# Performance work log

Hardware: AMD Instinct MI355X
Metric: run time of the kernel (lower is better)

The kernel has to match this reference:

```python
import jax, jax.numpy as jnp
import numpy as np

HEADS = 16

def setup_inputs() -> dict:
    key = jax.random.key(0)
    ks = jax.random.split(key, 5)
    B, T, D = 4, 2048, 1024
    scale = 0.02
    return {
        "x": jax.random.normal(ks[0], (B, T, D), dtype=jnp.float32),
        "W_attn": jax.random.normal(ks[1], (D, 3 * D), dtype=jnp.float32) * scale,
        "b_attn": jax.random.normal(ks[2], (3 * D,), dtype=jnp.float32) * scale,
        "W_proj": jax.random.normal(ks[3], (D, D), dtype=jnp.float32) * scale,
        "b_proj": jax.random.normal(ks[4], (D,), dtype=jnp.float32) * scale,
    }

def reference(x, W_attn, b_attn, W_proj, b_proj):
    B, T, D = x.shape
    H = HEADS
    hd = D // H
    qkv = x @ W_attn + b_attn                      # [B, T, 3D]
    q, k, v = jnp.split(qkv, 3, axis=2)
    # [B, T, H, hd] -> [B, H, T, hd]
    q = q.reshape(B, T, H, hd).transpose(0, 2, 1, 3)
    k = k.reshape(B, T, H, hd).transpose(0, 2, 1, 3)
    v = v.reshape(B, T, H, hd).transpose(0, 2, 1, 3)
    scale = hd ** 0.5
    scores = jnp.einsum("bhqd,bhkd->bhqk", q, k) / scale
    causal = jnp.tril(jnp.ones((T, T), dtype=bool))
    scores = jnp.where(causal, scores, -jnp.inf)
    attn = jax.nn.softmax(scores, axis=-1)
    out = jnp.einsum("bhqk,bhkd->bhqd", attn, v)    # [B, H, T, hd]
    out = out.transpose(0, 2, 1, 3).reshape(B, T, D)
    return out @ W_proj + b_proj
```

## Files before the change

kernel.cpp:

```cpp
#include <hip/hip_runtime.h>
#include <hip/hip_bf16.h>

using bf16 = __hip_bfloat16;
typedef __attribute__((ext_vector_type(8))) __bf16 bf16x8;
typedef __attribute__((ext_vector_type(4))) short s16x4;
typedef __attribute__((ext_vector_type(4))) float f32x4;

#define B_   4
#define T_   2048
#define D_   1024
#define H_   16
#define HD_  64
#define BH_  (B_ * H_)
#define BT_  (B_ * T_)

#define QSCALE 0.18033688011112042f

__device__ __forceinline__ void gld_lds16(const void* g, void* l) {
    __builtin_amdgcn_global_load_lds(
        (const __attribute__((address_space(1))) unsigned int*)g,
        (__attribute__((address_space(3))) unsigned int*)l,
        16, 0, 0);
}

__device__ __forceinline__ f32x4 mfma16(s16x4 a, s16x4 b, f32x4 c) {
#if defined(__HIP_DEVICE_COMPILE__)
  #if __has_builtin(__builtin_amdgcn_mfma_f32_16x16x16bf16_1k)
    return __builtin_amdgcn_mfma_f32_16x16x16bf16_1k(a, b, c, 0, 0, 0);
  #else
    f32x4 d;
    asm volatile("v_mfma_f32_16x16x16_bf16 %0, %1, %2, %3\n\ts_nop 7\n\ts_nop 7"
                 : "=v"(d) : "v"(a), "v"(b), "v"(c));
    return d;
  #endif
#else
    (void)a; (void)b;
    return c;
#endif
}

__device__ __forceinline__ unsigned bfbits(float x) {
    return (unsigned)__builtin_bit_cast(unsigned short, __float2bfloat16(x));
}

__global__ __launch_bounds__(256)
void prep_kernel(const float* __restrict__ x,
                 const float* __restrict__ W_attn,
                 const float* __restrict__ W_proj,
                 bf16* __restrict__ xh, bf16* __restrict__ WaT, bf16* __restrict__ WpT) {
    __shared__ float tile[32][33];
    const int blk = blockIdx.x;
    const int tid = threadIdx.x;

    if (blk < 4096) {
        const size_t i = ((size_t)blk * 256 + tid) * 8;
        float4 v0 = *reinterpret_cast<const float4*>(x + i);
        float4 v1 = *reinterpret_cast<const float4*>(x + i + 4);
        uint4 p;
        p.x = bfbits(v0.x) | (bfbits(v0.y) << 16);
        p.y = bfbits(v0.z) | (bfbits(v0.w) << 16);
        p.z = bfbits(v1.x) | (bfbits(v1.y) << 16);
        p.w = bfbits(v1.z) | (bfbits(v1.w) << 16);
        *reinterpret_cast<uint4*>(xh + i) = p;
        return;
    }

    const float* W;
    bf16* Wt;
    int nb, kb;
    if (blk < 4096 + 3072) {
        const int t = blk - 4096;
        W = W_attn; Wt = WaT;
        nb = (t % 96) * 32; kb = (t / 96) * 32;
        const int tx = tid & 31, ty = tid >> 5;
        #pragma unroll
        for (int i = 0; i < 32; i += 8)
            tile[ty + i][tx] = W[(size_t)(kb + ty + i) * 3072 + nb + tx];
        __syncthreads();
        #pragma unroll
        for (int i = 0; i < 32; i += 8)
            Wt[(size_t)(nb + ty + i) * 1024 + kb + tx] = __float2bfloat16(tile[tx][ty + i]);
    } else {
        const int t = blk - 4096 - 3072;
        W = W_proj; Wt = WpT;
        nb = (t % 32) * 32; kb = (t / 32) * 32;
        const int tx = tid & 31, ty = tid >> 5;
        #pragma unroll
        for (int i = 0; i < 32; i += 8)
            tile[ty + i][tx] = W[(size_t)(kb + ty + i) * 1024 + nb + tx];
        __syncthreads();
        #pragma unroll
        for (int i = 0; i < 32; i += 8)
            Wt[(size_t)(nb + ty + i) * 1024 + kb + tx] = __float2bfloat16(tile[tx][ty + i]);
    }
}

template <int MODE>
__global__ __launch_bounds__(256)
void gemm_bt(const bf16* __restrict__ A, const bf16* __restrict__ Bt,
             const float* __restrict__ bias,
             bf16* __restrict__ Qo, bf16* __restrict__ Ko, bf16* __restrict__ Vo,
             float* __restrict__ Fo) {
    constexpr int K = 1024;
    const int bm = blockIdx.x * 128;
    const int bn = blockIdx.y * 128;
    const int tid  = threadIdx.x;
    const int wid  = tid >> 6;
    const int lane = tid & 63;
    const int wr = (wid >> 1) * 64;
    const int wc = (wid & 1) * 64;
    const int ln_g = lane >> 4;
    const int ln_c = lane & 15;

    __shared__ bf16 sm[3][2][128][32];

    f32x4 acc[4][4] = {};

    const int g_row0 = wid * 32 + (lane >> 2);
    const int g_chk  = ((lane & 3) ^ ((lane >> 3) & 3)) * 8;
    const int l_row0 = wid * 32;
    const int colx = (ln_g * 16) ^ (((ln_c >> 1) & 3) << 4);

#define STAGE(S_, T_) {                                                               \
    gld_lds16(&A [(size_t)(bm + g_row0)      * K + (T_) * 32 + g_chk], &sm[S_][0][l_row0][0]);      \
    gld_lds16(&A [(size_t)(bm + g_row0 + 16) * K + (T_) * 32 + g_chk], &sm[S_][0][l_row0 + 16][0]); \
    gld_lds16(&Bt[(size_t)(bn + g_row0)      * K + (T_) * 32 + g_chk], &sm[S_][1][l_row0][0]);      \
    gld_lds16(&Bt[(size_t)(bn + g_row0 + 16) * K + (T_) * 32 + g_chk], &sm[S_][1][l_row0 + 16][0]); }

#define COMPUTE(S_) {                                                                    \
    bf16x8 af[4], bfr[4];                                                                \
    _Pragma("unroll")                                                                    \
    for (int m = 0; m < 4; ++m)                                                          \
        af[m] = *reinterpret_cast<const bf16x8*>(                                        \
            (const char*)&sm[S_][0][wr + m * 16 + ln_c][0] + colx);                      \
    _Pragma("unroll")                                                                    \
    for (int n = 0; n < 4; ++n)                                                          \
        bfr[n] = *reinterpret_cast<const bf16x8*>(                                       \
            (const char*)&sm[S_][1][wc + n * 16 + ln_c][0] + colx);                      \
    _Pragma("unroll")                                                                    \
    for (int m = 0; m < 4; ++m)                                                          \
        _Pragma("unroll")                                                                \
        for (int n = 0; n < 4; ++n)                                                      \
            acc[m][n] = __builtin_amdgcn_mfma_f32_16x16x32_bf16(af[m], bfr[n],           \
                                                                 acc[m][n], 0, 0, 0); }

#define WAITV4 { asm volatile("s_waitcnt vmcnt(4) lgkmcnt(0)" ::: "memory");             \
                 __builtin_amdgcn_s_barrier();                                           \
                 __builtin_amdgcn_sched_barrier(0); }
#define WAITV0 { asm volatile("s_waitcnt vmcnt(0) lgkmcnt(0)" ::: "memory");             \
                 __builtin_amdgcn_s_barrier();                                           \
                 __builtin_amdgcn_sched_barrier(0); }

    STAGE(0, 0);
    STAGE(1, 1);

    #pragma unroll 1
    for (int i = 0; i < 10; ++i) {
        const int t0 = i * 3;
        WAITV4; STAGE(2, t0 + 2); COMPUTE(0);
        WAITV4; STAGE(0, t0 + 3); COMPUTE(1);
        WAITV4; STAGE(1, t0 + 4); COMPUTE(2);
    }
    WAITV4; COMPUTE(0);
    WAITV0; COMPUTE(1);

#undef STAGE
#undef COMPUTE
#undef WAITV4
#undef WAITV0

    #pragma unroll
    for (int m = 0; m < 4; ++m) {
        #pragma unroll
        for (int n = 0; n < 4; ++n) {
            const int col = bn + wc + n * 16 + ln_c;
            const float bcol = bias[col];
            #pragma unroll
            for (int j = 0; j < 4; ++j) {
                const int row = bm + wr + m * 16 + ln_g * 4 + j;
                float v = acc[m][n][j] + bcol;
                if (MODE == 0) {
                    const int part = col >> 10;
                    const int cc = col & 1023;
                    const int h = cc >> 6, d = cc & 63;
                    const int b = row >> 11, t = row & 2047;
                    const int bh = b * H_ + h;
                    if (part == 0)
                        Qo[((size_t)bh * T_ + t) * HD_ + d] = __float2bfloat16(v * QSCALE);
                    else if (part == 1)
                        Ko[((size_t)bh * T_ + t) * HD_ + d] = __float2bfloat16(v);
                    else
                        Vo[((size_t)bh * HD_ + d) * T_ + t] = __float2bfloat16(v);
                } else {
                    Fo[(size_t)row * D_ + col] = v;
                }
            }
        }
    }
}

__global__ __launch_bounds__(256, 4)
void attn_kernel(const bf16* __restrict__ Q, const bf16* __restrict__ K,
                 const bf16* __restrict__ Vt, bf16* __restrict__ ctx) {
    const int bh = blockIdx.x & 63;
    const int qt = 31 - (blockIdx.x >> 6);
    const int tid  = threadIdx.x;
    const int wave = tid >> 6;
    const int lane = tid & 63;
    const int ln_g = lane >> 4;
    const int ln_c = lane & 15;

    const bf16* Qp = Q  + (size_t)bh * T_ * HD_;
    const bf16* Kp = K  + (size_t)bh * T_ * HD_;
    const bf16* Vp = Vt + (size_t)bh * HD_ * T_;

    __shared__ bf16 Ks[64][72];
    __shared__ bf16 Vs[64][72];

    const int srow = tid >> 3;
    const int sc8  = (tid & 7) * 8;

    const int b = bh >> 4, h = bh & 15;

    const int qbase = qt * 64;
    const int qglob = qbase + wave * 16 + ln_c;

    const bf16x8 qf0 = *reinterpret_cast<const bf16x8*>(&Qp[(size_t)qglob * HD_ + ln_g * 8]);
    const bf16x8 qf1 = *reinterpret_cast<const bf16x8*>(&Qp[(size_t)qglob * HD_ + 32 + ln_g * 8]);

    f32x4 o[4] = {};
    float m = -INFINITY, l = 0.f;

    const int nk = qt + 1;

    int4 kr0, kr1, vr0, vr1;
    kr0 = *reinterpret_cast<const int4*>(&Kp[(size_t)srow * HD_ + sc8]);
    kr1 = *reinterpret_cast<const int4*>(&Kp[(size_t)(srow + 32) * HD_ + sc8]);
    vr0 = *reinterpret_cast<const int4*>(&Vp[(size_t)srow * T_ + sc8]);
    vr1 = *reinterpret_cast<const int4*>(&Vp[(size_t)(srow + 32) * T_ + sc8]);
    *reinterpret_cast<int4*>(&Ks[srow][sc8])      = kr0;
    *reinterpret_cast<int4*>(&Ks[srow + 32][sc8]) = kr1;
    *reinterpret_cast<int4*>(&Vs[srow][sc8])      = vr0;
    *reinterpret_cast<int4*>(&Vs[srow + 32][sc8]) = vr1;
    __syncthreads();

    for (int it = 0; it < nk; ++it) {
        const int kb = it * 64;
        const bool notlast = (it + 1 < nk);
        if (notlast) {
            const int kn = kb + 64;
            kr0 = *reinterpret_cast<const int4*>(&Kp[(size_t)(kn + srow) * HD_ + sc8]);
            kr1 = *reinterpret_cast<const int4*>(&Kp[(size_t)(kn + srow + 32) * HD_ + sc8]);
            vr0 = *reinterpret_cast<const int4*>(&Vp[(size_t)srow * T_ + kn + sc8]);
            vr1 = *reinterpret_cast<const int4*>(&Vp[(size_t)(srow + 32) * T_ + kn + sc8]);
        }

        f32x4 st[4];
        __builtin_amdgcn_s_setprio(1);
        #pragma unroll
        for (int kk = 0; kk < 4; ++kk) {
            bf16x8 kfa = *reinterpret_cast<const bf16x8*>(&Ks[kk * 16 + ln_c][ln_g * 8]);
            bf16x8 kfb = *reinterpret_cast<const bf16x8*>(&Ks[kk * 16 + ln_c][32 + ln_g * 8]);
            f32x4 z = {0.f, 0.f, 0.f, 0.f};
            z = __builtin_amdgcn_mfma_f32_16x16x32_bf16(kfa, qf0, z, 0, 0, 0);
            z = __builtin_amdgcn_mfma_f32_16x16x32_bf16(kfb, qf1, z, 0, 0, 0);
            st[kk] = z;
        }
        __builtin_amdgcn_s_setprio(0);

        if (!notlast) {
            #pragma unroll
            for (int kk = 0; kk < 4; ++kk)
                #pragma unroll
                for (int j = 0; j < 4; ++j)
                    if (kb + kk * 16 + ln_g * 4 + j > qglob) st[kk][j] = -INFINITY;
        }

        float mx = -INFINITY;
        #pragma unroll
        for (int kk = 0; kk < 4; ++kk)
            #pragma unroll
            for (int j = 0; j < 4; ++j)
                mx = fmaxf(mx, st[kk][j]);
        if (!__all(mx - m <= 8.f)) {
            float r = fmaxf(mx, __shfl_xor(mx, 16));
            r = fmaxf(r, __shfl_xor(r, 32));
            const float mnew = fmaxf(m, r);
            const float alpha = exp2f(m - mnew);
            l *= alpha;
            #pragma unroll
            for (int dt = 0; dt < 4; ++dt)
                #pragma unroll
                for (int j = 0; j < 4; ++j)
                    o[dt][j] *= alpha;
            m = mnew;
        }

        #pragma unroll
        for (int kk = 0; kk < 4; ++kk) {
            float p0 = exp2f(st[kk][0] - m);
            float p1 = exp2f(st[kk][1] - m);
            float p2 = exp2f(st[kk][2] - m);
            float p3 = exp2f(st[kk][3] - m);
            l += (p0 + p1) + (p2 + p3);
            uint2 pw;
            pw.x = bfbits(p0) | (bfbits(p1) << 16);
            pw.y = bfbits(p2) | (bfbits(p3) << 16);
            const s16x4 ps = __builtin_bit_cast(s16x4, pw);
            __builtin_amdgcn_s_setprio(1);
            #pragma unroll
            for (int dt = 0; dt < 4; ++dt) {
                s16x4 vf = *reinterpret_cast<const s16x4*>(
                    &Vs[dt * 16 + ln_c][kk * 16 + ln_g * 4]);
                o[dt] = mfma16(vf, ps, o[dt]);
            }
            __builtin_amdgcn_s_setprio(0);
        }

        if (notlast) {
            __syncthreads();
            *reinterpret_cast<int4*>(&Ks[srow][sc8])      = kr0;
            *reinterpret_cast<int4*>(&Ks[srow + 32][sc8]) = kr1;
            *reinterpret_cast<int4*>(&Vs[srow][sc8])      = vr0;
            *reinterpret_cast<int4*>(&Vs[srow + 32][sc8]) = vr1;
            __syncthreads();
        }
    }

    l += __shfl_xor(l, 16);
    l += __shfl_xor(l, 32);
    const float inv = 1.0f / l;
    bf16* dst = ctx + ((size_t)(b * T_ + qglob)) * D_ + h * HD_;
    #pragma unroll
    for (int dt = 0; dt < 4; ++dt) {
        union { bf16 hh[4]; uint2 u; } ok;
        #pragma unroll
        for (int j = 0; j < 4; ++j)
            ok.hh[j] = __float2bfloat16(o[dt][j] * inv);
        *reinterpret_cast<uint2*>(&dst[dt * 16 + ln_g * 4]) = ok.u;
    }
}

extern "C" void kernel_launch(void* const* d_in, const int* in_sizes, int n_in,
                              void* d_out, int out_size, void* d_ws, size_t ws_size,
                              hipStream_t stream) {
    const float* x      = (const float*)d_in[0];
    const float* W_attn = (const float*)d_in[1];
    const float* b_attn = (const float*)d_in[2];
    const float* W_proj = (const float*)d_in[3];
    const float* b_proj = (const float*)d_in[4];
    float* out = (float*)d_out;

    char* ws = (char*)d_ws;
    bf16* xh  = (bf16*)ws;  ws += (size_t)BT_ * D_ * 2;
    bf16* WaT = (bf16*)ws;  ws += (size_t)3 * D_ * D_ * 2;
    bf16* WpT = (bf16*)ws;  ws += (size_t)D_ * D_ * 2;
    bf16* Qb  = (bf16*)ws;  ws += (size_t)BH_ * T_ * HD_ * 2;
    bf16* Kb  = (bf16*)ws;  ws += (size_t)BH_ * T_ * HD_ * 2;
    bf16* Vb  = (bf16*)ws;  ws += (size_t)BH_ * T_ * HD_ * 2;
    bf16* ctx = (bf16*)ws;  ws += (size_t)BT_ * D_ * 2;

    prep_kernel<<<8192, 256, 0, stream>>>(x, W_attn, W_proj, xh, WaT, WpT);

    gemm_bt<0><<<dim3(BT_ / 128, 3 * D_ / 128), 256, 0, stream>>>(
        xh, WaT, b_attn, Qb, Kb, Vb, nullptr);

    attn_kernel<<<dim3(BH_ * 32), 256, 0, stream>>>(Qb, Kb, Vb, ctx);

    gemm_bt<1><<<dim3(BT_ / 128, D_ / 128), 256, 0, stream>>>(
        ctx, WpT, b_proj, nullptr, nullptr, nullptr, out);
}
```

Measured before the change: 180.1 us.

## Replace QKV GEMM with 256x256-tile 8-wave ping-pong pipelined kernel

The QKV projection GEMM moves from the generic 128x128 templated kernel to a dedicated 512-thread kernel with 256x256 tiles. It uses 128KB of dynamic LDS holding two buffers, loads through global_load_lds with an XOR swizzle, and runs a hand-scheduled phase pipeline built from explicit waitcnt, barriers and setprio. The intent is more data reuse per tile and better overlap of loads with MFMA work. The cost is large LDS use, so each CU can hold fewer blocks. The fragile manual vmcnt accounting risks hazards, and the grid has only 384 blocks, which can leave load imbalance across CUs.

```diff
diff --git a/kernel.cpp b/kernel.cpp
--- a/kernel.cpp
+++ b/kernel.cpp
@@ -65,42 +65,167 @@
         return;
     }
 
-    const float* W;
-    bf16* Wt;
-    int nb, kb;
     if (blk < 4096 + 3072) {
         const int t = blk - 4096;
-        W = W_attn; Wt = WaT;
-        nb = (t % 96) * 32; kb = (t / 96) * 32;
+        const int nb = (t % 96) * 32, kb = (t / 96) * 32;
         const int tx = tid & 31, ty = tid >> 5;
         #pragma unroll
         for (int i = 0; i < 32; i += 8)
-            tile[ty + i][tx] = W[(size_t)(kb + ty + i) * 3072 + nb + tx];
+            tile[ty + i][tx] = W_attn[(size_t)(kb + ty + i) * 3072 + nb + tx];
         __syncthreads();
         #pragma unroll
         for (int i = 0; i < 32; i += 8)
-            Wt[(size_t)(nb + ty + i) * 1024 + kb + tx] = __float2bfloat16(tile[tx][ty + i]);
+            WaT[(size_t)(nb + ty + i) * 1024 + kb + tx] = __float2bfloat16(tile[tx][ty + i]);
     } else {
         const int t = blk - 4096 - 3072;
-        W = W_proj; Wt = WpT;
-        nb = (t % 32) * 32; kb = (t / 32) * 32;
+        const int nb = (t % 32) * 32, kb = (t / 32) * 32;
         const int tx = tid & 31, ty = tid >> 5;
         #pragma unroll
         for (int i = 0; i < 32; i += 8)
-            tile[ty + i][tx] = W[(size_t)(kb + ty + i) * 1024 + nb + tx];
+            tile[ty + i][tx] = W_proj[(size_t)(kb + ty + i) * 1024 + nb + tx];
         __syncthreads();
         #pragma unroll
         for (int i = 0; i < 32; i += 8)
-            Wt[(size_t)(nb + ty + i) * 1024 + kb + tx] = __float2bfloat16(tile[tx][ty + i]);
-    }
-}
-
-template <int MODE>
+            WpT[(size_t)(nb + ty + i) * 1024 + kb + tx] = __float2bfloat16(tile[tx][ty + i]);
+    }
+}
+
+__global__ __launch_bounds__(512, 2)
+void gemm_qkv8p(const bf16* __restrict__ Ap, const bf16* __restrict__ Bp,
+                const float* __restrict__ bias,
+                bf16* __restrict__ Qo, bf16* __restrict__ Ko, bf16* __restrict__ Vo) {
+    extern __shared__ char smem[];
+    const int bn = blockIdx.x * 256;
+    const int bm = blockIdx.y * 256;
+    const int tid  = threadIdx.x;
+    const int wid  = tid >> 6;
+    const int lane = tid & 63;
+    const int wr = (wid >> 2) * 128;
+    const int wc = (wid & 3) * 64;
+    const int ln_g = lane >> 4;
+    const int ln_c = lane & 15;
+
+    f32x4 acc[8][4] = {};
+    bf16x8 brg[4][2];
+
+    const int srw = wid * 8 + (lane >> 3);
+    const int gck = ((lane & 7) ^ ((lane >> 3) & 7)) * 8;
+    const int wlo = wid * 1024;
+
+    const int c0 = ((ln_g)     ^ (ln_c & 7)) * 16;
+    const int c1 = ((4 + ln_g) ^ (ln_c & 7)) * 16;
+
+#define GA(T_, J_, BO_) gld_lds16(Ap + (size_t)(bm + (J_) * 64 + srw) * 1024 + (T_) * 64 + gck, \
+                                  smem + (BO_) + (J_) * 8192 + wlo)
+#define GB(T_, J_, BO_) gld_lds16(Bp + (size_t)(bn + (J_) * 64 + srw) * 1024 + (T_) * 64 + gck, \
+                                  smem + (BO_) + 32768 + (J_) * 8192 + wlo)
+#define SB01(T_, BO_) { GB(T_, 0, BO_); GB(T_, 1, BO_); }
+#define SB23(T_, BO_) { GB(T_, 2, BO_); GB(T_, 3, BO_); }
+#define SA02(T_, BO_) { GA(T_, 0, BO_); GA(T_, 2, BO_); }
+#define SA13(T_, BO_) { GA(T_, 1, BO_); GA(T_, 3, BO_); }
+#define NOSTG {}
+
+#define PH(BO_, Q0_, RB_, STG_, VM_) {                                                    \
+    const char* aB_ = smem + (BO_) + (wr + ln_c) * 128;                                   \
+    const char* bB_ = smem + (BO_) + 32768 + (wc + ln_c) * 128;                           \
+    bf16x8 a_[2][2];                                                                      \
+    _Pragma("unroll")                                                                     \
+    for (int dm = 0; dm < 2; ++dm) {                                                      \
+        a_[dm][0] = *(const bf16x8*)(aB_ + ((Q0_) * 2 + dm) * 2048 + c0);                 \
+        a_[dm][1] = *(const bf16x8*)(aB_ + ((Q0_) * 2 + dm) * 2048 + c1);                 \
+    }                                                                                     \
+    if (RB_) {                                                                            \
+        _Pragma("unroll")                                                                 \
+        for (int n = 0; n < 4; ++n) {                                                     \
+            brg[n][0] = *(const bf16x8*)(bB_ + n * 2048 + c0);                            \
+            brg[n][1] = *(const bf16x8*)(bB_ + n * 2048 + c1);                            \
+        }                                                                                 \
+    }                                                                                     \
+    STG_;                                                                                 \
+    __builtin_amdgcn_s_barrier();                                                         \
+    asm volatile("s_waitcnt lgkmcnt(0)" ::: "memory");                                    \
+    __builtin_amdgcn_sched_barrier(0);                                                    \
+    __builtin_amdgcn_s_setprio(1);                                                        \
+    _Pragma("unroll")                                                                     \
+    for (int dm = 0; dm < 2; ++dm)                                                        \
+        _Pragma("unroll")                                                                 \
+        for (int n = 0; n < 4; ++n) {                                                     \
+            acc[(Q0_) * 2 + dm][n] = __builtin_amdgcn_mfma_f32_16x16x32_bf16(             \
+                a_[dm][0], brg[n][0], acc[(Q0_) * 2 + dm][n], 0, 0, 0);                   \
+            acc[(Q0_) * 2 + dm][n] = __builtin_amdgcn_mfma_f32_16x16x32_bf16(             \
+                a_[dm][1], brg[n][1], acc[(Q0_) * 2 + dm][n], 0, 0, 0);                   \
+        }                                                                                 \
+    __builtin_amdgcn_s_setprio(0);                                                        \
+    __builtin_amdgcn_sched_barrier(0);                                                    \
+    asm volatile("s_waitcnt vmcnt(" #VM_ ")" ::: "memory");                               \
+    __builtin_amdgcn_s_barrier();                                                         \
+}
+
+    SB01(0, 0); SB23(0, 0); SA02(0, 0); SA13(0, 0);
+    SB01(1, 65536); SB23(1, 65536); SA02(1, 65536); SA13(1, 65536);
+    asm volatile("s_waitcnt vmcnt(10)" ::: "memory");
+    __builtin_amdgcn_s_barrier();
+    __builtin_amdgcn_sched_barrier(0);
+
+    #pragma unroll 1
+    for (int i = 0; i < 7; ++i) {
+        const int t0 = 2 * i;
+        PH(0,     0, 1, { if (i) SA13(t0 + 1, 65536); }, 10)
+        PH(0,     1, 0, SB01(t0 + 2, 0),      10)
+        PH(0,     2, 0, SB23(t0 + 2, 0),      12)
+        PH(0,     3, 0, SA02(t0 + 2, 0),      8)
+        PH(65536, 0, 1, SA13(t0 + 2, 0),      10)
+        PH(65536, 1, 0, SB01(t0 + 3, 65536),  10)
+        PH(65536, 2, 0, SB23(t0 + 3, 65536),  12)
+        PH(65536, 3, 0, SA02(t0 + 3, 65536),  8)
+    }
+    PH(0,     0, 1, SA13(15, 65536), 10)
+    PH(0,     1, 0, NOSTG, 8)
+    PH(0,     2, 0, NOSTG, 8)
+    PH(0,     3, 0, NOSTG, 2)
+    PH(65536, 0, 1, NOSTG, 2)
+    PH(65536, 1, 0, NOSTG, 0)
+    PH(65536, 2, 0, NOSTG, 0)
+    PH(65536, 3, 0, NOSTG, 0)
+
+#undef PH
+#undef GA
+#undef GB
+#undef SB01
+#undef SB23
+#undef SA02
+#undef SA13
+#undef NOSTG
+
+    #pragma unroll
+    for (int m = 0; m < 8; ++m) {
+        #pragma unroll
+        for (int n = 0; n < 4; ++n) {
+            const int col = bn + wc + n * 16 + ln_c;
+            const float bcol = bias[col];
+            #pragma unroll
+            for (int j = 0; j < 4; ++j) {
+                const int row = bm + wr + m * 16 + ln_g * 4 + j;
+                float v = acc[m][n][j] + bcol;
+                const int part = col >> 10;
+                const int cc = col & 1023;
+                const int h = cc >> 6, d = cc & 63;
+                const int b = row >> 11, t = row & 2047;
+                const int bh = b * H_ + h;
+                if (part == 0)
+                    Qo[((size_t)bh * T_ + t) * HD_ + d] = __float2bfloat16(v * QSCALE);
+                else if (part == 1)
+                    Ko[((size_t)bh * T_ + t) * HD_ + d] = __float2bfloat16(v);
+                else
+                    Vo[((size_t)bh * HD_ + d) * T_ + t] = __float2bfloat16(v);
+            }
+        }
+    }
+}
+
 __global__ __launch_bounds__(256)
-void gemm_bt(const bf16* __restrict__ A, const bf16* __restrict__ Bt,
-             const float* __restrict__ bias,
-             bf16* __restrict__ Qo, bf16* __restrict__ Ko, bf16* __restrict__ Vo,
-             float* __restrict__ Fo) {
+void gemm_proj(const bf16* __restrict__ A, const bf16* __restrict__ Bt,
+               const float* __restrict__ bias, float* __restrict__ Fo) {
     constexpr int K = 1024;
     const int bm = blockIdx.x * 128;
     const int bn = blockIdx.y * 128;
@@ -178,22 +303,7 @@
             #pragma unroll
             for (int j = 0; j < 4; ++j) {
                 const int row = bm + wr + m * 16 + ln_g * 4 + j;
-                float v = acc[m][n][j] + bcol;
-                if (MODE == 0) {
-                    const int part = col >> 10;
-                    const int cc = col & 1023;
-                    const int h = cc >> 6, d = cc & 63;
-                    const int b = row >> 11, t = row & 2047;
-                    const int bh = b * H_ + h;
-                    if (part == 0)
-                        Qo[((size_t)bh * T_ + t) * HD_ + d] = __float2bfloat16(v * QSCALE);
-                    else if (part == 1)
-                        Ko[((size_t)bh * T_ + t) * HD_ + d] = __float2bfloat16(v);
-                    else
-                        Vo[((size_t)bh * HD_ + d) * T_ + t] = __float2bfloat16(v);
-                } else {
-                    Fo[(size_t)row * D_ + col] = v;
-                }
+                Fo[(size_t)row * D_ + col] = acc[m][n][j] + bcol;
             }
         }
     }
@@ -362,11 +472,9 @@
 
     prep_kernel<<<8192, 256, 0, stream>>>(x, W_attn, W_proj, xh, WaT, WpT);
 
-    gemm_bt<0><<<dim3(BT_ / 128, 3 * D_ / 128), 256, 0, stream>>>(
-        xh, WaT, b_attn, Qb, Kb, Vb, nullptr);
+    gemm_qkv8p<<<dim3(12, 32), 512, 131072, stream>>>(xh, WaT, b_attn, Qb, Kb, Vb);
 
     attn_kernel<<<dim3(BH_ * 32), 256, 0, stream>>>(Qb, Kb, Vb, ctx);
 
-    gemm_bt<1><<<dim3(BT_ / 128, D_ / 128), 256, 0, stream>>>(
-        ctx, WpT, b_proj, nullptr, nullptr, nullptr, out);
-}
+    gemm_proj<<<dim3(64, 8), 256, 0, stream>>>(ctx, WpT, b_proj, out);
+}
```

New measurement: 189.5 us. 1.05x slower.
